# Performance work log

Hardware: AMD Instinct MI355X
Metric: run time of the kernel (lower is better)

The kernel has to match this reference:

```python
import jax, jax.numpy as jnp
import numpy as np

B = 1
H_IMG, W_IMG = 64, 64
NF = H_IMG * W_IMG          # 4096 front/query tokens
NS = 1024                   # satellite tokens (32x32 grid)
SAT_IN, FRONT_IN = 768, 320
NH, HD = 8, 64
MD = NH * HD                # 512
GHID, GHD = 128, 16
GMD = NH * GHD              # 128
GEO_RATIO, ROPE_BASE = 0.5, 10000.0
LAMBDA_GEO, LAMBDA_GEOM = 1.0, 1.0
EPS = 1e-5


def _linear(x, w, b):
    return x @ w.T + b


def _layernorm(x, g, b):
    m = x.mean(-1, keepdims=True)
    v = jnp.var(x, axis=-1, keepdims=True)
    return (x - m) / jnp.sqrt(v + EPS) * g + b


def _georope(t, xy):
    """Continuous 2D (x,y) rotary embedding on the first GEO_RATIO fraction of head_dim.
    t: [B,NH,N,HD], xy: [B,N,2]."""
    rot = int(HD * GEO_RATIO)       # rotated dims (32)
    axis = rot // 2                 # dims per spatial axis (16)
    half = axis // 2                # frequency pairs per axis (8)
    inv_freq = ROPE_BASE ** (-jnp.arange(half, dtype=t.dtype) / half)

    def rot_axis(a, coord):
        th = coord[:, None, :, None] * inv_freq   # [B,1,N,half]
        c, s = jnp.cos(th), jnp.sin(th)
        a1, a2 = a[..., :half], a[..., half:]
        return jnp.concatenate([a1 * c - a2 * s, a1 * s + a2 * c], axis=-1)

    tx = rot_axis(t[..., :axis], xy[..., 0])
    ty = rot_axis(t[..., axis:rot], xy[..., 1])
    return jnp.concatenate([tx, ty, t[..., rot:]], axis=-1)


def _heads(x, hd):
    b, n, _ = x.shape
    return x.reshape(b, n, NH, hd).transpose(0, 2, 1, 3)


def setup_inputs() -> dict:
    key = jax.random.key(0)
    ks = iter(jax.random.split(key, 64))

    def w(*shape):
        return jax.random.normal(next(ks), shape, jnp.float32) / np.sqrt(shape[-1]).astype(np.float32)

    z = lambda n: jnp.zeros((n,), jnp.float32)
    o = lambda n: jnp.ones((n,), jnp.float32)
    return {
        "front_feat": jax.random.normal(next(ks), (B, FRONT_IN, H_IMG, W_IMG), jnp.float32),
        "front_bev_xy": jax.random.uniform(next(ks), (B, NF, 2), jnp.float32, -1.0, 1.0),
        "sat_tokens": jax.random.normal(next(ks), (B, NS, SAT_IN), jnp.float32),
        "sat_xy": jax.random.uniform(next(ks), (B, NS, 2), jnp.float32, -1.0, 1.0),
        "front_plucker": jax.random.normal(next(ks), (B, NF, 6), jnp.float32),
        "pos_w1": w(MD, 2), "pos_b1": z(MD), "pos_w2": w(MD, MD), "pos_b2": z(MD),
        "fa_w": w(MD, FRONT_IN), "fa_b": z(MD), "fa_ln_g": o(MD), "fa_ln_b": z(MD),
        "qn_g": o(MD), "qn_b": z(MD),
        "sa_w": w(MD, SAT_IN), "sa_b": z(MD), "sa_ln_g": o(MD), "sa_ln_b": z(MD),
        "wq": w(MD, MD), "bq": z(MD), "wk": w(MD, MD), "bk": z(MD), "wv": w(MD, MD), "bv": z(MD),
        "plk_w1": w(GHID, 6), "plk_b1": z(GHID), "plk_w2": w(GHID, GHID), "plk_b2": z(GHID),
        "sxy_w1": w(GHID, 2), "sxy_b1": z(GHID), "sxy_w2": w(GHID, GHID), "sxy_b2": z(GHID),
        "gqn_g": o(GHID), "gqn_b": z(GHID), "gkn_g": o(GHID), "gkn_b": z(GHID),
        "wqg": w(GMD, GHID), "bqg": z(GMD), "wkg": w(GMD, GHID), "bkg": z(GMD),
    }


def reference(front_feat, front_bev_xy, sat_tokens, sat_xy, front_plucker,
              pos_w1, pos_b1, pos_w2, pos_b2, fa_w, fa_b, fa_ln_g, fa_ln_b,
              qn_g, qn_b, sa_w, sa_b, sa_ln_g, sa_ln_b, wq, bq, wk, bk, wv, bv,
              plk_w1, plk_b1, plk_w2, plk_b2, sxy_w1, sxy_b1, sxy_w2, sxy_b2,
              gqn_g, gqn_b, gkn_g, gkn_b, wqg, bqg, wkg, bkg):
    b = front_feat.shape[0]
    ff = front_feat.reshape(b, FRONT_IN, NF).transpose(0, 2, 1)      # [B,NF,C]
    pos = _linear(jax.nn.silu(_linear(front_bev_xy, pos_w1, pos_b1)), pos_w2, pos_b2)
    feat = _layernorm(_linear(ff, fa_w, fa_b), fa_ln_g, fa_ln_b)
    q_embed = _layernorm(pos + feat, qn_g, qn_b)
    sat_feat = _layernorm(_linear(sat_tokens, sa_w, sa_b), sa_ln_g, sa_ln_b)
    q = _heads(_linear(q_embed, wq, bq), HD)                         # [B,H,NF,HD]
    k = _heads(_linear(sat_feat, wk, bk), HD)                        # [B,H,NS,HD]
    v = _heads(_linear(sat_feat, wv, bv), HD)
    qr = _georope(q, front_bev_xy)
    kr = _georope(k, sat_xy)
    logits = jnp.einsum('bhqd,bhkd->bhqk', qr, kr) / np.float32(np.sqrt(HD))
    # learned geometric Q/K stream (Plucker rays vs sat xy)
    plk = _layernorm(_linear(jax.nn.silu(_linear(front_plucker, plk_w1, plk_b1)), plk_w2, plk_b2), gqn_g, gqn_b)
    sgf = _layernorm(_linear(jax.nn.silu(_linear(sat_xy, sxy_w1, sxy_b1)), sxy_w2, sxy_b2), gkn_g, gkn_b)
    qg = _heads(_linear(plk, wqg, bqg), GHD)
    kg = _heads(_linear(sgf, wkg, bkg), GHD)
    logits = logits + LAMBDA_GEOM * (jnp.einsum('bhqd,bhkd->bhqk', qg, kg) / np.float32(np.sqrt(GHD)))
    # additive pairwise squared-distance bias, broadcast over heads
    dist2 = ((front_bev_xy[:, :, None, :] - sat_xy[:, None, :, :]) ** 2).sum(-1)   # [B,NF,NS]
    logits = logits - LAMBDA_GEO * dist2[:, None]
    attn = jax.nn.softmax(logits, axis=-1)
    read = jnp.einsum('bhqk,bhkd->bhqd', attn, v)
    return read.transpose(0, 2, 1, 3).reshape(b, NF, MD)
```

## Files before the change

### kernel.cpp

```cpp
#include <hip/hip_runtime.h>
#include <hip/hip_bf16.h>
#include <stdint.h>

#define NF 4096
#define NS 1024
#define MD 512
#define HD 64
#define DA 96
#define GHID 128

#define L2E 1.44269504f
#define S2L 1.6986436f
#define SMAX 12.0f

typedef unsigned short u16;
typedef __attribute__((ext_vector_type(8))) short bf8v;
typedef __attribute__((ext_vector_type(4))) float f4v;

__device__ __forceinline__ u16 f2bf(float f) {
  __hip_bfloat16 h = __float2bfloat16(f);
  return __builtin_bit_cast(u16, h);
}
__device__ __forceinline__ float bf2f(u16 u) {
  union { unsigned u; float f; } v; v.u = ((unsigned)u) << 16; return v.f;
}
__device__ __forceinline__ f4v mfma16(bf8v a, bf8v b, f4v c) {
  return __builtin_amdgcn_mfma_f32_16x16x32_bf16(a, b, c, 0, 0, 0);
}
__device__ __forceinline__ void gld16(const void* g, void* l) {
  __builtin_amdgcn_global_load_lds(
      (const __attribute__((address_space(1))) unsigned int*)g,
      (__attribute__((address_space(3))) unsigned int*)l, 16, 0, 0);
}

#define OFF_POSW2 0
#define OFF_FAW   262144
#define OFF_SAW   425984
#define OFF_WQ    819200
#define OFF_WKV   1081344
#define OFF_PLKW2 1605632
#define OFF_SXYW2 1622016
#define OFF_WQG   1638400
#define OFF_WKG   1654784
#define OFF_SATT  1671168
#define TOTW      2457600

__global__ __launch_bounds__(256) void k_l0(
    const float* __restrict__ s0, const float* __restrict__ s1,
    const float* __restrict__ s2, const float* __restrict__ s3,
    const float* __restrict__ s4, const float* __restrict__ s5,
    const float* __restrict__ s6, const float* __restrict__ s7,
    const float* __restrict__ s8, const float* __restrict__ s9,
    const float* __restrict__ s10, u16* __restrict__ pool,
    const float* __restrict__ bk, const float* __restrict__ bv,
    float* __restrict__ bkv,
    const float* __restrict__ ff, u16* __restrict__ ffT,
    const float* __restrict__ in0, const float* __restrict__ w0,
    const float* __restrict__ b0, u16* __restrict__ o0,
    const float* __restrict__ in1, const float* __restrict__ w1,
    const float* __restrict__ b1, u16* __restrict__ o1,
    const float* __restrict__ in2, const float* __restrict__ w2,
    const float* __restrict__ b2, u16* __restrict__ o2) {
  __shared__ u16 sT[32][72];
  int blk = blockIdx.x, t = threadIdx.x;
  if (blk < 2401) {
    int i4 = blk * 256 + t;
    if (i4 < TOTW / 4) {
      int idx = i4 * 4;
      const float* src; int off;
      if      (idx < OFF_FAW)   { src = s0;  off = OFF_POSW2; }
      else if (idx < OFF_SAW)   { src = s1;  off = OFF_FAW; }
      else if (idx < OFF_WQ)    { src = s2;  off = OFF_SAW; }
      else if (idx < OFF_WKV)   { src = s3;  off = OFF_WQ; }
      else if (idx < 1343488)   { src = s4;  off = OFF_WKV; }
      else if (idx < OFF_PLKW2) { src = s5;  off = 1343488; }
      else if (idx < OFF_SXYW2) { src = s6;  off = OFF_PLKW2; }
      else if (idx < OFF_WQG)   { src = s7;  off = OFF_SXYW2; }
      else if (idx < OFF_WKG)   { src = s8;  off = OFF_WQG; }
      else if (idx < OFF_SATT)  { src = s9;  off = OFF_WKG; }
      else                      { src = s10; off = OFF_SATT; }
      float4 v = *(const float4*)(src + (idx - off));
      ushort4 o;
      o.x = f2bf(v.x); o.y = f2bf(v.y); o.z = f2bf(v.z); o.w = f2bf(v.w);
      *(ushort4*)(pool + idx) = o;
    } else if (i4 < TOTW / 4 + 256) {
      int j = (i4 - TOTW / 4) * 4;
#pragma unroll
      for (int e = 0; e < 4; ++e) {
        int b = j + e;
        bkv[b] = (b < 512) ? bk[b] : bv[b - 512];
      }
    }
  } else if (blk < 3041) {
    int lb = blk - 2401;
    int n0 = (lb & 63) * 64, c0 = (lb >> 6) * 32;
    {
      int cr = t >> 3, nc = (t & 7) * 8;
      const float* src = ff + (size_t)(c0 + cr) * NF + n0 + nc;
      float4 v0 = *(const float4*)src, v1 = *(const float4*)(src + 4);
      bf8v p;
      p[0]=(short)f2bf(v0.x); p[1]=(short)f2bf(v0.y); p[2]=(short)f2bf(v0.z); p[3]=(short)f2bf(v0.w);
      p[4]=(short)f2bf(v1.x); p[5]=(short)f2bf(v1.y); p[6]=(short)f2bf(v1.z); p[7]=(short)f2bf(v1.w);
      *(bf8v*)&sT[cr][nc] = p;
    }
    __syncthreads();
    {
      int r = t >> 2, cc = (t & 3) * 8;
      bf8v p;
#pragma unroll
      for (int e = 0; e < 8; ++e) p[e] = (short)sT[cc + e][r];
      *(bf8v*)(ffT + (size_t)(n0 + r) * 320 + c0 + cc) = p;
    }
  } else {
    int lb = blk - 3041;
    const float *in, *w, *b; u16* o; int mlog, K, idx;
    if (lb < 8192)       { in = in0; w = w0; b = b0; o = o0; mlog = 9; K = 2; idx = lb * 256 + t; }
    else if (lb < 10240) { in = in1; w = w1; b = b1; o = o1; mlog = 7; K = 6; idx = (lb - 8192) * 256 + t; }
    else                 { in = in2; w = w2; b = b2; o = o2; mlog = 7; K = 2; idx = (lb - 10240) * 256 + t; }
    int M = 1 << mlog;
    int n = idx >> mlog, m = idx & (M - 1);
    float acc = b[m];
    for (int k = 0; k < K; ++k) acc += in[n * K + k] * w[m * K + k];
    o[idx] = f2bf(acc / (1.f + __expf(-acc)));
  }
}

__device__ __forceinline__ void gemm_body(const u16* __restrict__ A, const u16* __restrict__ W,
                                          const float* __restrict__ bias, u16* __restrict__ out,
                                          int m0, int n0, int N, int K) {
  constexpr int BM = 64, BN = 64;
  constexpr int MR = 2, NR = 2;
  __shared__ u16 sA[2][BM * 64];
  __shared__ u16 sB[2][BN * 64];
  const int tid = threadIdx.x, w = tid >> 6, lane = tid & 63;
  const int l16 = lane & 15, lh = lane >> 4;
  const int wr = w >> 1, wc = w & 1;

  f4v acc[MR][NR];
#pragma unroll
  for (int m = 0; m < MR; ++m)
#pragma unroll
    for (int j = 0; j < NR; ++j) acc[m][j] = (f4v){0.f, 0.f, 0.f, 0.f};

  auto stageA = [&](int buf, int k0) {
#pragma unroll
    for (int i = 0; i < 2; ++i) {
      int c = i * 256 + tid;
      int row = c >> 3, cp = c & 7;
      int sc_ = cp ^ (row & 7);
      gld16(A + (size_t)(m0 + row) * K + k0 + sc_ * 8, &sA[buf][c * 8]);
    }
  };
  auto stageB = [&](int buf, int k0) {
#pragma unroll
    for (int i = 0; i < 2; ++i) {
      int c = i * 256 + tid;
      int row = c >> 3, cp = c & 7;
      int sc_ = cp ^ (row & 7);
      gld16(W + (size_t)(n0 + row) * K + k0 + sc_ * 8, &sB[buf][c * 8]);
    }
  };

  stageA(0, 0); stageB(0, 0);
  __syncthreads();
  const int NK = K >> 6;
  for (int ks = 0; ks < NK; ++ks) {
    int nb = ks & 1;
    if (ks + 1 < NK) { stageA(nb ^ 1, (ks + 1) * 64); stageB(nb ^ 1, (ks + 1) * 64); }
#pragma unroll
    for (int kk = 0; kk < 2; ++kk) {
      bf8v af[MR], bfr[NR];
#pragma unroll
      for (int m = 0; m < MR; ++m) {
        int row = wr * 32 + m * 16 + l16;
        int cp = (kk * 4 + lh) ^ (row & 7);
        af[m] = *(const bf8v*)&sA[nb][row * 64 + cp * 8];
      }
#pragma unroll
      for (int j = 0; j < NR; ++j) {
        int row = wc * 32 + j * 16 + l16;
        int cp = (kk * 4 + lh) ^ (row & 7);
        bfr[j] = *(const bf8v*)&sB[nb][row * 64 + cp * 8];
      }
#pragma unroll
      for (int m = 0; m < MR; ++m)
#pragma unroll
        for (int j = 0; j < NR; ++j) acc[m][j] = mfma16(af[m], bfr[j], acc[m][j]);
    }
    __syncthreads();
  }
#pragma unroll
  for (int m = 0; m < MR; ++m) {
    int grow = m0 + wr * 32 + m * 16 + (lh << 2);
#pragma unroll
    for (int j = 0; j < NR; ++j) {
      int gcol = n0 + wc * 32 + j * 16 + l16;
      float bv = bias ? bias[gcol] : 0.f;
#pragma unroll
      for (int r = 0; r < 4; ++r)
        out[(size_t)(grow + r) * N + gcol] = f2bf(acc[m][j][r] + bv);
    }
  }
}

struct GP { const u16* A; const u16* W; const float* bias; u16* out; int K; int N; int M; };

__device__ __forceinline__ void gemm_dispatch(const GP& g, int blk) {
  int mt = g.M >> 6;
  int m0 = (blk % mt) * 64, n0 = (blk / mt) * 64;
  gemm_body(g.A, g.W, g.bias, g.out, m0, n0, g.N, g.K);
}

__global__ __launch_bounds__(256) void k_gemm_L1(GP a, GP b, GP c, GP d, GP e) {
  int blk = blockIdx.x;
  if (blk < 512)       gemm_dispatch(a, blk);
  else if (blk < 1024) gemm_dispatch(b, blk - 512);
  else if (blk < 1152) gemm_dispatch(c, blk - 1024);
  else if (blk < 1280) gemm_dispatch(d, blk - 1152);
  else                 gemm_dispatch(e, blk - 1280);
}
__global__ __launch_bounds__(256) void k_gemm_L2(GP a, GP b, GP c, GP d) {
  int blk = blockIdx.x;
  if (blk < 512)      gemm_dispatch(a, blk);
  else if (blk < 768) gemm_dispatch(b, blk - 512);
  else if (blk < 896) gemm_dispatch(c, blk - 768);
  else                gemm_dispatch(d, blk - 896);
}

__global__ __launch_bounds__(256) void k_ln_all(
    const u16* __restrict__ feat_pre, const u16* __restrict__ pos,
    const float* __restrict__ fg, const float* __restrict__ fb,
    const float* __restrict__ qg, const float* __restrict__ qb2,
    u16* __restrict__ q_embed,
    const u16* __restrict__ satf_pre, const float* __restrict__ sg,
    const float* __restrict__ sb, u16* __restrict__ satf,
    const u16* __restrict__ ginq, const u16* __restrict__ gink,
    const float* __restrict__ ggq, const float* __restrict__ gbq,
    const float* __restrict__ ggk, const float* __restrict__ gbk,
    u16* __restrict__ goutq, u16* __restrict__ goutk) {
  int blk = blockIdx.x;
  int w = threadIdx.x >> 6, lane = threadIdx.x & 63;
  if (blk < 1024) {
    int row = blk * 4 + w;
    bf8v v = *(const bf8v*)(feat_pre + (size_t)row * 512 + lane * 8);
    float x[8];
#pragma unroll
    for (int e = 0; e < 8; ++e) x[e] = bf2f((u16)v[e]);
    float s = 0.f, q = 0.f;
#pragma unroll
    for (int e = 0; e < 8; ++e) { s += x[e]; q += x[e] * x[e]; }
#pragma unroll
    for (int mm = 1; mm < 64; mm <<= 1) { s += __shfl_xor(s, mm); q += __shfl_xor(q, mm); }
    float mean = s / 512.f, var = q / 512.f - mean * mean;
    float rstd = rsqrtf(var + 1e-5f);
    bf8v vp = *(const bf8v*)(pos + (size_t)row * 512 + lane * 8);
#pragma unroll
    for (int e = 0; e < 8; ++e)
      x[e] = (x[e] - mean) * rstd * fg[lane * 8 + e] + fb[lane * 8 + e] + bf2f((u16)vp[e]);
    s = 0.f; q = 0.f;
#pragma unroll
    for (int e = 0; e < 8; ++e) { s += x[e]; q += x[e] * x[e]; }
#pragma unroll
    for (int mm = 1; mm < 64; mm <<= 1) { s += __shfl_xor(s, mm); q += __shfl_xor(q, mm); }
    mean = s / 512.f; var = q / 512.f - mean * mean;
    rstd = rsqrtf(var + 1e-5f);
    bf8v ov;
#pragma unroll
    for (int e = 0; e < 8; ++e)
      ov[e] = (short)f2bf((x[e] - mean) * rstd * qg[lane * 8 + e] + qb2[lane * 8 + e]);
    *(bf8v*)(q_embed + (size_t)row * 512 + lane * 8) = ov;
  } else if (blk < 1280) {
    int row = (blk - 1024) * 4 + w;
    bf8v v = *(const bf8v*)(satf_pre + (size_t)row * 512 + lane * 8);
    float x[8];
#pragma unroll
    for (int e = 0; e < 8; ++e) x[e] = bf2f((u16)v[e]);
    float s = 0.f, q = 0.f;
#pragma unroll
    for (int e = 0; e < 8; ++e) { s += x[e]; q += x[e] * x[e]; }
#pragma unroll
    for (int mm = 1; mm < 64; mm <<= 1) { s += __shfl_xor(s, mm); q += __shfl_xor(q, mm); }
    float mean = s / 512.f, var = q / 512.f - mean * mean;
    float rstd = rsqrtf(var + 1e-5f);
    bf8v ov;
#pragma unroll
    for (int e = 0; e < 8; ++e)
      ov[e] = (short)f2bf((x[e] - mean) * rstd * sg[lane * 8 + e] + sb[lane * 8 + e]);
    *(bf8v*)(satf + (size_t)row * 512 + lane * 8) = ov;
  } else {
    int row = (blk - 1280) * 4 + w;
    const u16* in; const float *g, *b; u16* out;
    if (row < 4096) { in = ginq; g = ggq; b = gbq; out = goutq; }
    else { row -= 4096; in = gink; g = ggk; b = gbk; out = goutk; }
    uint32_t v = *(const uint32_t*)(in + (size_t)row * 128 + lane * 2);
    float x0 = bf2f((u16)(v & 0xffff)), x1 = bf2f((u16)(v >> 16));
    float s = x0 + x1, q = x0 * x0 + x1 * x1;
#pragma unroll
    for (int mm = 1; mm < 64; mm <<= 1) { s += __shfl_xor(s, mm); q += __shfl_xor(q, mm); }
    float mean = s / 128.f, var = q / 128.f - mean * mean;
    float rstd = rsqrtf(var + 1e-5f);
    u16 o0 = f2bf((x0 - mean) * rstd * g[lane * 2] + b[lane * 2]);
    u16 o1 = f2bf((x1 - mean) * rstd * g[lane * 2 + 1] + b[lane * 2 + 1]);
    *(uint32_t*)(out + (size_t)row * 128 + lane * 2) = (uint32_t)o0 | ((uint32_t)o1 << 16);
  }
}

__global__ __launch_bounds__(256) void k_prep(
    const u16* __restrict__ qlin, const u16* __restrict__ qglin,
    const float* __restrict__ qxy, u16* __restrict__ Qaug_,
    const u16* __restrict__ klin, const u16* __restrict__ kglin,
    const float* __restrict__ kxy, u16* __restrict__ Kaug_,
    float* __restrict__ kk2_, u16* __restrict__ VT) {
  __shared__ u16 sT[64][72];
  int blk = blockIdx.x;
  if (blk < 10240) {
    int gid = blk * 4 + (threadIdx.x >> 6);
    int lane = threadIdx.x & 63;
    const u16 *lin, *glin; const float* xy; u16* aug;
    int lstride, n, h, isQ; float scm, scg;
    if (gid < NF * 8) {
      lin = qlin; glin = qglin; xy = qxy; aug = Qaug_;
      lstride = MD; n = gid >> 3; h = gid & 7; isQ = 1;
      scm = 0.125f * L2E; scg = 0.25f * L2E;
    } else {
      gid -= NF * 8;
      lin = klin; glin = kglin; xy = kxy; aug = Kaug_;
      lstride = 1024; n = gid >> 3; h = gid & 7; isQ = 0;
      scm = 1.f; scg = 1.f;
    }
    float val = bf2f(lin[(size_t)n * lstride + h * 64 + lane]);
    float part = __shfl_xor(val, 8);
    float x = xy[n * 2], y = xy[n * 2 + 1];
    float outv = val;
    if (lane < 32) {
      float coord = (lane < 16) ? x : y;
      int j = lane & 7;
      float th = coord * __expf(-(float)j * 1.1512925465f);
      float sn, cs;
      __sincosf(th, &sn, &cs);
      outv = ((lane & 8) == 0) ? (val * cs - part * sn) : (part * sn + val * cs);
    }
    u16* dst = aug + (size_t)(h * (isQ ? NF : NS) + n) * DA;
    dst[lane] = f2bf(outv * scm);
    if (lane < 16) {
      float gv = bf2f(glin[(size_t)n * GHID + h * 16 + lane]);
      dst[64 + lane] = f2bf(gv * scg);
    } else if (lane == 16) {
      dst[80] = f2bf(S2L * x);
    } else if (lane == 17) {
      dst[81] = f2bf(S2L * y);
    } else if (lane == 18) {
      dst[82] = 0;
      if (!isQ && h == 0) kk2_[n] = L2E * (x * x + y * y) + SMAX;
    } else if (lane < 32) {
      dst[64 + lane] = 0;
    }
  } else {
    int lb = blk - 10240;
    int n0 = (lb & 15) * 64, h = lb >> 4;
    int t = threadIdx.x;
    int r = t >> 2, c = (t & 3) * 16;
    const u16* src = klin + (size_t)(n0 + r) * 1024 + 512 + h * 64 + c;
    *(bf8v*)&sT[r][c]     = *(const bf8v*)src;
    *(bf8v*)&sT[r][c + 8] = *(const bf8v*)(src + 8);
    __syncthreads();
    int d = t >> 2, nc = (t & 3) * 16;
    bf8v p0, p1;
#pragma unroll
    for (int e = 0; e < 8; ++e) { p0[e] = (short)sT[nc + e][d]; p1[e] = (short)sT[nc + 8 + e][d]; }
    u16* dst = VT + (size_t)(h * 64 + d) * 1024 + n0 + nc;
    *(bf8v*)dst = p0;
    *(bf8v*)(dst + 8) = p1;
  }
}

__global__ __launch_bounds__(256, 4) void k_flash(const u16* __restrict__ Qa,
                                                  const u16* __restrict__ Ka,
                                                  const u16* __restrict__ VT,
                                                  const float* __restrict__ kk2,
                                                  float* __restrict__ Opart,
                                                  float* __restrict__ lbuf) {
  const int h = blockIdx.y, qb = blockIdx.x, sp = blockIdx.z;
  const int tid = threadIdx.x, w = tid >> 6, lane = tid & 63;
  const int l16 = lane & 15, lh = lane >> 4;
  __shared__ u16 sK[64][104];
  __shared__ u16 sV[64][72];
  __shared__ u16 sP[4][16][72];
  __shared__ float sKK[512];

  ((float2*)sKK)[tid] = ((const float2*)(kk2 + sp * 512))[tid];

  const int qrow = qb * 64 + w * 16 + l16;
  bf8v qf[3];
#pragma unroll
  for (int c = 0; c < 3; ++c)
    qf[c] = *(const bf8v*)(Qa + (size_t)(h * NF + qrow) * DA + c * 32 + lh * 8);

  bf8v ONES;
#pragma unroll
  for (int i = 0; i < 8; ++i) ONES[i] = (short)0x3F80;

  const int crow = qb * 64 + w * 16 + (lh << 2);
  float l_run[4] = {0.f, 0.f, 0.f, 0.f};
  f4v accO[4];
#pragma unroll
  for (int d = 0; d < 4; ++d) accO[d] = (f4v){0.f, 0.f, 0.f, 0.f};

  const int kt0 = sp * 8;
  bf8v kreg[3], vreg[2];
  auto sload = [&](int t8) {
    int kb = (kt0 + t8) * 64;
#pragma unroll
    for (int i = 0; i < 3; ++i) {
      int c = tid + i * 256; int r = c / 12, off = (c % 12) * 8;
      kreg[i] = *(const bf8v*)(Ka + ((size_t)(h * NS) + kb + r) * DA + off);
    }
#pragma unroll
    for (int i = 0; i < 2; ++i) {
      int c = tid + i * 256; int d = c >> 3, off = (c & 7) * 8;
      vreg[i] = *(const bf8v*)(VT + ((size_t)(h * HD) + d) * NS + kb + off);
    }
  };
  auto swrite = [&]() {
#pragma unroll
    for (int i = 0; i < 3; ++i) {
      int c = tid + i * 256; int r = c / 12, off = (c % 12) * 8;
      *(bf8v*)&sK[r][off] = kreg[i];
    }
#pragma unroll
    for (int i = 0; i < 2; ++i) {
      int c = tid + i * 256; int d = c >> 3, off = (c & 7) * 8;
      *(bf8v*)&sV[d][off] = vreg[i];
    }
  };

  sload(0); swrite();
  __syncthreads();
  for (int t8 = 0; t8 < 8; ++t8) {
    if (t8 < 7) sload(t8 + 1);
#pragma unroll
    for (int j = 0; j < 4; ++j) {
      f4v s4 = (f4v){0.f, 0.f, 0.f, 0.f};
#pragma unroll
      for (int c = 0; c < 3; ++c) {
        bf8v kf = *(const bf8v*)&sK[j * 16 + l16][c * 32 + lh * 8];
        s4 = mfma16(qf[c], kf, s4);
      }
      float ck = sKK[t8 * 64 + j * 16 + l16];
#pragma unroll
      for (int r = 0; r < 4; ++r) {
        float pv = exp2f(s4[r] - ck);
        sP[w][(lh << 2) + r][j * 16 + l16] = f2bf(pv);
      }
    }
    bf8v pf0 = *(const bf8v*)&sP[w][l16][lh * 8];
    bf8v pf1 = *(const bf8v*)&sP[w][l16][32 + lh * 8];
    f4v ls = (f4v){0.f, 0.f, 0.f, 0.f};
    ls = mfma16(pf0, ONES, ls);
    ls = mfma16(pf1, ONES, ls);
#pragma unroll
    for (int r = 0; r < 4; ++r) l_run[r] += ls[r];
#pragma unroll
    for (int c = 0; c < 2; ++c) {
      bf8v pf = (c == 0) ? pf0 : pf1;
#pragma unroll
      for (int d = 0; d < 4; ++d) {
        bf8v vf = *(const bf8v*)&sV[d * 16 + l16][c * 32 + lh * 8];
        accO[d] = mfma16(pf, vf, accO[d]);
      }
    }
    __syncthreads();
    if (t8 < 7) swrite();
    __syncthreads();
  }
  size_t obase = (size_t)(sp * 8 + h) * NF + crow;
#pragma unroll
  for (int d = 0; d < 4; ++d)
#pragma unroll
    for (int r = 0; r < 4; ++r)
      Opart[(obase + r) * 64 + d * 16 + l16] = accO[d][r];
  if (l16 == 0) {
#pragma unroll
    for (int r = 0; r < 4; ++r) lbuf[obase + r] = l_run[r];
  }
}

__global__ void k_combine(const float* __restrict__ Opart, const float* __restrict__ lbuf,
                          float* __restrict__ out) {
  int i4 = blockIdx.x * 256 + threadIdx.x;
  int n = i4 >> 7;
  int c4 = i4 & 127, h = c4 >> 4, d4 = c4 & 15;
  float l = lbuf[(size_t)h * NF + n] + lbuf[(size_t)(8 + h) * NF + n];
  float rl = 1.f / l;
  float4 o1 = ((const float4*)(Opart + ((size_t)h * NF + n) * 64))[d4];
  float4 o2 = ((const float4*)(Opart + ((size_t)(8 + h) * NF + n) * 64))[d4];
  float4 r;
  r.x = (o1.x + o2.x) * rl;
  r.y = (o1.y + o2.y) * rl;
  r.z = (o1.z + o2.z) * rl;
  r.w = (o1.w + o2.w) * rl;
  ((float4*)out)[i4] = r;
}

extern "C" void kernel_launch(void* const* d_in, const int* in_sizes, int n_in,
                              void* d_out, int out_size, void* d_ws, size_t ws_size,
                              hipStream_t stream) {
  (void)in_sizes; (void)n_in; (void)out_size; (void)ws_size;
  const float* front_feat = (const float*)d_in[0];
  const float* bev_xy     = (const float*)d_in[1];
  const float* sat_tokens = (const float*)d_in[2];
  const float* sat_xy     = (const float*)d_in[3];
  const float* plucker    = (const float*)d_in[4];
  const float* pos_w1 = (const float*)d_in[5];
  const float* pos_b1 = (const float*)d_in[6];
  const float* pos_w2 = (const float*)d_in[7];
  const float* pos_b2 = (const float*)d_in[8];
  const float* fa_w   = (const float*)d_in[9];
  const float* fa_b   = (const float*)d_in[10];
  const float* fa_ln_g = (const float*)d_in[11];
  const float* fa_ln_b = (const float*)d_in[12];
  const float* qn_g   = (const float*)d_in[13];
  const float* qn_b   = (const float*)d_in[14];
  const float* sa_w   = (const float*)d_in[15];
  const float* sa_b   = (const float*)d_in[16];
  const float* sa_ln_g = (const float*)d_in[17];
  const float* sa_ln_b = (const float*)d_in[18];
  const float* wq = (const float*)d_in[19];
  const float* bq = (const float*)d_in[20];
  const float* wk = (const float*)d_in[21];
  const float* bk = (const float*)d_in[22];
  const float* wv = (const float*)d_in[23];
  const float* bv = (const float*)d_in[24];
  const float* plk_w1 = (const float*)d_in[25];
  const float* plk_b1 = (const float*)d_in[26];
  const float* plk_w2 = (const float*)d_in[27];
  const float* plk_b2 = (const float*)d_in[28];
  const float* sxy_w1 = (const float*)d_in[29];
  const float* sxy_b1 = (const float*)d_in[30];
  const float* sxy_w2 = (const float*)d_in[31];
  const float* sxy_b2 = (const float*)d_in[32];
  const float* gqn_g = (const float*)d_in[33];
  const float* gqn_b = (const float*)d_in[34];
  const float* gkn_g = (const float*)d_in[35];
  const float* gkn_b = (const float*)d_in[36];
  const float* wqg = (const float*)d_in[37];
  const float* bqg = (const float*)d_in[38];
  const float* wkg = (const float*)d_in[39];
  const float* bkg = (const float*)d_in[40];

  char* ws = (char*)d_ws;
  size_t off = 0;
  auto alloc = [&](size_t bytes) {
    size_t r = off;
    off += (bytes + 255) & ~(size_t)255;
    return r;
  };
  u16*   wpool   = (u16*)(ws + alloc((size_t)TOTW * 2));
  float* bkv     = (float*)(ws + alloc(1024 * 4));
  u16*   ffT     = (u16*)(ws + alloc((size_t)NF * 320 * 2));
  u16*   pos_h   = (u16*)(ws + alloc((size_t)NF * MD * 2));
  u16*   plk_h   = (u16*)(ws + alloc((size_t)NF * GHID * 2));
  u16*   sxy_h   = (u16*)(ws + alloc((size_t)NS * GHID * 2));
  u16*   pos     = (u16*)(ws + alloc((size_t)NF * MD * 2));
  u16*   feat_pre= (u16*)(ws + alloc((size_t)NF * MD * 2));
  u16*   satf_pre= (u16*)(ws + alloc((size_t)NS * MD * 2));
  u16*   satf    = (u16*)(ws + alloc((size_t)NS * MD * 2));
  u16*   q_embed = (u16*)(ws + alloc((size_t)NF * MD * 2));
  u16*   plk2    = (u16*)(ws + alloc((size_t)NF * GHID * 2));
  u16*   sxy2    = (u16*)(ws + alloc((size_t)NS * GHID * 2));
  u16*   q_lin   = (u16*)(ws + alloc((size_t)NF * MD * 2));
  u16*   kv_lin  = (u16*)(ws + alloc((size_t)NS * 1024 * 2));
  u16*   Qaug    = (u16*)(ws + alloc((size_t)8 * NF * DA * 2));
  u16*   Kaug    = (u16*)(ws + alloc((size_t)8 * NS * DA * 2));
  u16*   VT      = (u16*)(ws + alloc((size_t)8 * HD * NS * 2));
  float* kk2     = (float*)(ws + alloc((size_t)NS * 4));
  float* Opart   = (float*)(ws + alloc((size_t)2 * 8 * NF * 64 * 4));
  float* lbuf    = (float*)(ws + alloc((size_t)2 * 8 * NF * 4));
  u16* plk_ln = plk_h;
  u16* sgf    = sxy_h;
  u16* qg_lin = plk2;
  u16* kg_lin = sxy2;

  dim3 b256(256);
  k_l0<<<dim3(13793), b256, 0, stream>>>(
      pos_w2, fa_w, sa_w, wq, wk, wv, plk_w2, sxy_w2, wqg, wkg, sat_tokens,
      wpool, bk, bv, bkv, front_feat, ffT,
      bev_xy, pos_w1, pos_b1, pos_h,
      plucker, plk_w1, plk_b1, plk_h,
      sat_xy, sxy_w1, sxy_b1, sxy_h);

  GP gpos {pos_h, wpool + OFF_POSW2, pos_b2, pos, 512, 512, 4096};
  GP gfeat{ffT, wpool + OFF_FAW, fa_b, feat_pre, 320, 512, 4096};
  GP gsat {wpool + OFF_SATT, wpool + OFF_SAW, sa_b, satf_pre, 768, 512, 1024};
  GP ggq1 {plk_h, wpool + OFF_PLKW2, plk_b2, plk2, 128, 128, 4096};
  GP ggk1 {sxy_h, wpool + OFF_SXYW2, sxy_b2, sxy2, 128, 128, 1024};
  k_gemm_L1<<<dim3(1312), b256, 0, stream>>>(gpos, gfeat, gsat, ggq1, ggk1);

  k_ln_all<<<dim3(2560), b256, 0, stream>>>(
      feat_pre, pos, fa_ln_g, fa_ln_b, qn_g, qn_b, q_embed,
      satf_pre, sa_ln_g, sa_ln_b, satf,
      plk2, sxy2, gqn_g, gqn_b, gkn_g, gkn_b, plk_ln, sgf);

  GP gq  {q_embed, wpool + OFF_WQ, bq, q_lin, 512, 512, 4096};
  GP gkv {satf, wpool + OFF_WKV, bkv, kv_lin, 512, 1024, 1024};
  GP ggq2{plk_ln, wpool + OFF_WQG, bqg, qg_lin, 128, 128, 4096};
  GP ggk2{sgf, wpool + OFF_WKG, bkg, kg_lin, 128, 128, 1024};
  k_gemm_L2<<<dim3(928), b256, 0, stream>>>(gq, gkv, ggq2, ggk2);

  k_prep<<<dim3(10368), b256, 0, stream>>>(
      q_lin, qg_lin, bev_xy, Qaug, kv_lin, kg_lin, sat_xy, Kaug, kk2, VT);

  k_flash<<<dim3(NF / 64, 8, 2), b256, 0, stream>>>(Qaug, Kaug, VT, kk2, Opart, lbuf);
  k_combine<<<dim3(NF * MD / 4 / 256), b256, 0, stream>>>(Opart, lbuf, (float*)d_out);
}
```

Baseline: 87.01 us.

## Fuse RoPE/Qaug/Kaug/VT prep into GEMM epilogues and store split-K partials in bf16

Removes the k_prep kernel. The geo-rope rotation, scaling, Qaug/Kaug packing and the V transpose now happen directly in the L2 GEMM epilogues, and the constant xy/zero columns plus kk2 are written by extra blocks in the first kernel. This drops one launch and the round trip of the q_lin/kv_lin intermediates through memory. Separately, the flash kernel's split partial outputs are stored as bf16 instead of fp32, which halves combine traffic but loses some precision. The epilogue stores become scattered, with per-element writes into strided aug buffers.

Result: faster. 79.76 us (-8.3%).

```diff
diff --git a/kernel.cpp b/kernel.cpp
--- a/kernel.cpp
+++ b/kernel.cpp
@@ -44,6 +44,11 @@
 #define OFF_WKG   1654784
 #define OFF_SATT  1671168
 #define TOTW      2457600
+
+#define EPI_OUT  0
+#define EPI_ROPE 1
+#define EPI_VT   2
+#define EPI_GEO  3
 
 __global__ __launch_bounds__(256) void k_l0(
     const float* __restrict__ s0, const float* __restrict__ s1,
@@ -60,7 +65,8 @@
     const float* __restrict__ in1, const float* __restrict__ w1,
     const float* __restrict__ b1, u16* __restrict__ o1,
     const float* __restrict__ in2, const float* __restrict__ w2,
-    const float* __restrict__ b2, u16* __restrict__ o2) {
+    const float* __restrict__ b2, u16* __restrict__ o2,
+    u16* __restrict__ Qaug, u16* __restrict__ Kaug, float* __restrict__ kk2) {
   __shared__ u16 sT[32][72];
   int blk = blockIdx.x, t = threadIdx.x;
   if (blk < 2401) {
@@ -111,7 +117,7 @@
       for (int e = 0; e < 8; ++e) p[e] = (short)sT[cc + e][r];
       *(bf8v*)(ffT + (size_t)(n0 + r) * 320 + c0 + cc) = p;
     }
-  } else {
+  } else if (blk < 13793) {
     int lb = blk - 3041;
     const float *in, *w, *b; u16* o; int mlog, K, idx;
     if (lb < 8192)       { in = in0; w = w0; b = b0; o = o0; mlog = 9; K = 2; idx = lb * 256 + t; }
@@ -122,16 +128,35 @@
     float acc = b[m];
     for (int k = 0; k < K; ++k) acc += in[n * K + k] * w[m * K + k];
     o[idx] = f2bf(acc / (1.f + __expf(-acc)));
+  } else {
+    int id = (blk - 13793) * 256 + t;
+    int side = id >= NF * 8;
+    int lid = side ? id - NF * 8 : id;
+    int n = lid >> 3, h = lid & 7;
+    const float* xy = side ? in2 : in0;
+    u16* aug = side ? Kaug : Qaug;
+    int nrows = side ? NS : NF;
+    float x = xy[n * 2], y = xy[n * 2 + 1];
+    bf8v p0, z;
+#pragma unroll
+    for (int e = 0; e < 8; ++e) { p0[e] = 0; z[e] = 0; }
+    p0[0] = (short)f2bf(S2L * x);
+    p0[1] = (short)f2bf(S2L * y);
+    u16* dst = aug + ((size_t)h * nrows + n) * DA + 80;
+    *(bf8v*)dst = p0;
+    *(bf8v*)(dst + 8) = z;
+    if (side && h == 0) kk2[n] = L2E * (x * x + y * y) + SMAX;
   }
 }
 
 __device__ __forceinline__ void gemm_body(const u16* __restrict__ A, const u16* __restrict__ W,
                                           const float* __restrict__ bias, u16* __restrict__ out,
-                                          int m0, int n0, int N, int K) {
-  constexpr int BM = 64, BN = 64;
+                                          int m0, int n0, int N, int K,
+                                          int mode, float scale, const float* __restrict__ xy,
+                                          u16* __restrict__ aug, int nrows) {
   constexpr int MR = 2, NR = 2;
-  __shared__ u16 sA[2][BM * 64];
-  __shared__ u16 sB[2][BN * 64];
+  __shared__ u16 sA[2][64 * 64];
+  __shared__ u16 sB[2][64 * 64];
   const int tid = threadIdx.x, w = tid >> 6, lane = tid & 63;
   const int l16 = lane & 15, lh = lane >> 4;
   const int wr = w >> 1, wc = w & 1;
@@ -189,26 +214,91 @@
     }
     __syncthreads();
   }
-#pragma unroll
-  for (int m = 0; m < MR; ++m) {
-    int grow = m0 + wr * 32 + m * 16 + (lh << 2);
-#pragma unroll
-    for (int j = 0; j < NR; ++j) {
-      int gcol = n0 + wc * 32 + j * 16 + l16;
-      float bv = bias ? bias[gcol] : 0.f;
-#pragma unroll
-      for (int r = 0; r < 4; ++r)
-        out[(size_t)(grow + r) * N + gcol] = f2bf(acc[m][j][r] + bv);
+
+  if (mode == EPI_OUT) {
+#pragma unroll
+    for (int m = 0; m < MR; ++m) {
+      int grow = m0 + wr * 32 + m * 16 + (lh << 2);
+#pragma unroll
+      for (int j = 0; j < NR; ++j) {
+        int gcol = n0 + wc * 32 + j * 16 + l16;
+        float bvs = bias ? bias[gcol] : 0.f;
+#pragma unroll
+        for (int r = 0; r < 4; ++r)
+          out[(size_t)(grow + r) * N + gcol] = f2bf(acc[m][j][r] + bvs);
+      }
+    }
+  } else if (mode == EPI_ROPE) {
+    float fr = __expf(-(float)(l16 & 7) * 1.1512925465f);
+#pragma unroll
+    for (int m = 0; m < MR; ++m) {
+      int grow = m0 + wr * 32 + m * 16 + (lh << 2);
+#pragma unroll
+      for (int j = 0; j < NR; ++j) {
+        int gcol = n0 + wc * 32 + j * 16 + l16;
+        int h = gcol >> 6, d = gcol & 63;
+        float bvs = bias[gcol];
+#pragma unroll
+        for (int r = 0; r < 4; ++r) {
+          int n = grow + r;
+          float val = acc[m][j][r] + bvs;
+          float part = __shfl_xor(val, 8);
+          float outv = val;
+          if (wc == 0) {
+            float2 c2 = ((const float2*)xy)[n];
+            float coord = j ? c2.y : c2.x;
+            float sn, cs;
+            __sincosf(coord * fr, &sn, &cs);
+            outv = (l16 & 8) ? (part * sn + val * cs) : (val * cs - part * sn);
+          }
+          aug[((size_t)h * nrows + n) * DA + d] = f2bf(outv * scale);
+        }
+      }
+    }
+  } else if (mode == EPI_VT) {
+#pragma unroll
+    for (int m = 0; m < MR; ++m) {
+      int grow = m0 + wr * 32 + m * 16 + (lh << 2);
+#pragma unroll
+      for (int j = 0; j < NR; ++j) {
+        int gcol = n0 + wc * 32 + j * 16 + l16;
+        int vcol = gcol - 512;
+        int h = vcol >> 6, d = vcol & 63;
+        float bvs = bias[gcol];
+        ushort4 o;
+        o.x = f2bf(acc[m][j][0] + bvs);
+        o.y = f2bf(acc[m][j][1] + bvs);
+        o.z = f2bf(acc[m][j][2] + bvs);
+        o.w = f2bf(acc[m][j][3] + bvs);
+        *(ushort4*)(aug + ((size_t)(h * 64 + d)) * NS + grow) = o;
+      }
+    }
+  } else {
+#pragma unroll
+    for (int m = 0; m < MR; ++m) {
+      int grow = m0 + wr * 32 + m * 16 + (lh << 2);
+#pragma unroll
+      for (int j = 0; j < NR; ++j) {
+        int gcol = n0 + wc * 32 + j * 16 + l16;
+        int h = gcol >> 4, dg = gcol & 15;
+        float bvs = bias[gcol];
+#pragma unroll
+        for (int r = 0; r < 4; ++r)
+          aug[((size_t)h * nrows + grow + r) * DA + 64 + dg] = f2bf((acc[m][j][r] + bvs) * scale);
+      }
     }
   }
 }
 
-struct GP { const u16* A; const u16* W; const float* bias; u16* out; int K; int N; int M; };
+struct GP { const u16* A; const u16* W; const float* bias; u16* out;
+            int K; int N; int M; int mode; float scale; const float* xy;
+            u16* aug; int nrows; };
 
 __device__ __forceinline__ void gemm_dispatch(const GP& g, int blk) {
   int mt = g.M >> 6;
   int m0 = (blk % mt) * 64, n0 = (blk / mt) * 64;
-  gemm_body(g.A, g.W, g.bias, g.out, m0, n0, g.N, g.K);
+  gemm_body(g.A, g.W, g.bias, g.out, m0, n0, g.N, g.K,
+            g.mode, g.scale, g.xy, g.aug, g.nrows);
 }
 
 __global__ __launch_bounds__(256) void k_gemm_L1(GP a, GP b, GP c, GP d, GP e) {
@@ -219,12 +309,22 @@
   else if (blk < 1280) gemm_dispatch(d, blk - 1152);
   else                 gemm_dispatch(e, blk - 1280);
 }
-__global__ __launch_bounds__(256) void k_gemm_L2(GP a, GP b, GP c, GP d) {
+__global__ __launch_bounds__(256) void k_gemm_L2(GP a, GP b, GP c, GP d, u16* VTp) {
   int blk = blockIdx.x;
-  if (blk < 512)      gemm_dispatch(a, blk);
-  else if (blk < 768) gemm_dispatch(b, blk - 512);
-  else if (blk < 896) gemm_dispatch(c, blk - 768);
-  else                gemm_dispatch(d, blk - 896);
+  if (blk < 512) {
+    gemm_dispatch(a, blk);
+  } else if (blk < 768) {
+    int lb = blk - 512;
+    int m0 = (lb & 15) * 64, n0 = (lb >> 4) * 64;
+    if (n0 >= 512)
+      gemm_body(b.A, b.W, b.bias, b.out, m0, n0, b.N, b.K, EPI_VT, 1.f, nullptr, VTp, NS);
+    else
+      gemm_body(b.A, b.W, b.bias, b.out, m0, n0, b.N, b.K, b.mode, b.scale, b.xy, b.aug, b.nrows);
+  } else if (blk < 896) {
+    gemm_dispatch(c, blk - 768);
+  } else {
+    gemm_dispatch(d, blk - 896);
+  }
 }
 
 __global__ __launch_bounds__(256) void k_ln_all(
@@ -305,80 +405,11 @@
   }
 }
 
-__global__ __launch_bounds__(256) void k_prep(
-    const u16* __restrict__ qlin, const u16* __restrict__ qglin,
-    const float* __restrict__ qxy, u16* __restrict__ Qaug_,
-    const u16* __restrict__ klin, const u16* __restrict__ kglin,
-    const float* __restrict__ kxy, u16* __restrict__ Kaug_,
-    float* __restrict__ kk2_, u16* __restrict__ VT) {
-  __shared__ u16 sT[64][72];
-  int blk = blockIdx.x;
-  if (blk < 10240) {
-    int gid = blk * 4 + (threadIdx.x >> 6);
-    int lane = threadIdx.x & 63;
-    const u16 *lin, *glin; const float* xy; u16* aug;
-    int lstride, n, h, isQ; float scm, scg;
-    if (gid < NF * 8) {
-      lin = qlin; glin = qglin; xy = qxy; aug = Qaug_;
-      lstride = MD; n = gid >> 3; h = gid & 7; isQ = 1;
-      scm = 0.125f * L2E; scg = 0.25f * L2E;
-    } else {
-      gid -= NF * 8;
-      lin = klin; glin = kglin; xy = kxy; aug = Kaug_;
-      lstride = 1024; n = gid >> 3; h = gid & 7; isQ = 0;
-      scm = 1.f; scg = 1.f;
-    }
-    float val = bf2f(lin[(size_t)n * lstride + h * 64 + lane]);
-    float part = __shfl_xor(val, 8);
-    float x = xy[n * 2], y = xy[n * 2 + 1];
-    float outv = val;
-    if (lane < 32) {
-      float coord = (lane < 16) ? x : y;
-      int j = lane & 7;
-      float th = coord * __expf(-(float)j * 1.1512925465f);
-      float sn, cs;
-      __sincosf(th, &sn, &cs);
-      outv = ((lane & 8) == 0) ? (val * cs - part * sn) : (part * sn + val * cs);
-    }
-    u16* dst = aug + (size_t)(h * (isQ ? NF : NS) + n) * DA;
-    dst[lane] = f2bf(outv * scm);
-    if (lane < 16) {
-      float gv = bf2f(glin[(size_t)n * GHID + h * 16 + lane]);
-      dst[64 + lane] = f2bf(gv * scg);
-    } else if (lane == 16) {
-      dst[80] = f2bf(S2L * x);
-    } else if (lane == 17) {
-      dst[81] = f2bf(S2L * y);
-    } else if (lane == 18) {
-      dst[82] = 0;
-      if (!isQ && h == 0) kk2_[n] = L2E * (x * x + y * y) + SMAX;
-    } else if (lane < 32) {
-      dst[64 + lane] = 0;
-    }
-  } else {
-    int lb = blk - 10240;
-    int n0 = (lb & 15) * 64, h = lb >> 4;
-    int t = threadIdx.x;
-    int r = t >> 2, c = (t & 3) * 16;
-    const u16* src = klin + (size_t)(n0 + r) * 1024 + 512 + h * 64 + c;
-    *(bf8v*)&sT[r][c]     = *(const bf8v*)src;
-    *(bf8v*)&sT[r][c + 8] = *(const bf8v*)(src + 8);
-    __syncthreads();
-    int d = t >> 2, nc = (t & 3) * 16;
-    bf8v p0, p1;
-#pragma unroll
-    for (int e = 0; e < 8; ++e) { p0[e] = (short)sT[nc + e][d]; p1[e] = (short)sT[nc + 8 + e][d]; }
-    u16* dst = VT + (size_t)(h * 64 + d) * 1024 + n0 + nc;
-    *(bf8v*)dst = p0;
-    *(bf8v*)(dst + 8) = p1;
-  }
-}
-
 __global__ __launch_bounds__(256, 4) void k_flash(const u16* __restrict__ Qa,
                                                   const u16* __restrict__ Ka,
                                                   const u16* __restrict__ VT,
                                                   const float* __restrict__ kk2,
-                                                  float* __restrict__ Opart,
+                                                  u16* __restrict__ Opart,
                                                   float* __restrict__ lbuf) {
   const int h = blockIdx.y, qb = blockIdx.x, sp = blockIdx.z;
   const int tid = threadIdx.x, w = tid >> 6, lane = tid & 63;
@@ -478,27 +509,27 @@
   for (int d = 0; d < 4; ++d)
 #pragma unroll
     for (int r = 0; r < 4; ++r)
-      Opart[(obase + r) * 64 + d * 16 + l16] = accO[d][r];
+      Opart[(obase + r) * 64 + d * 16 + l16] = f2bf(accO[d][r]);
   if (l16 == 0) {
 #pragma unroll
     for (int r = 0; r < 4; ++r) lbuf[obase + r] = l_run[r];
   }
 }
 
-__global__ void k_combine(const float* __restrict__ Opart, const float* __restrict__ lbuf,
+__global__ void k_combine(const u16* __restrict__ Opart, const float* __restrict__ lbuf,
                           float* __restrict__ out) {
   int i4 = blockIdx.x * 256 + threadIdx.x;
   int n = i4 >> 7;
   int c4 = i4 & 127, h = c4 >> 4, d4 = c4 & 15;
   float l = lbuf[(size_t)h * NF + n] + lbuf[(size_t)(8 + h) * NF + n];
   float rl = 1.f / l;
-  float4 o1 = ((const float4*)(Opart + ((size_t)h * NF + n) * 64))[d4];
-  float4 o2 = ((const float4*)(Opart + ((size_t)(8 + h) * NF + n) * 64))[d4];
+  ushort4 a = ((const ushort4*)(Opart + ((size_t)h * NF + n) * 64))[d4];
+  ushort4 b = ((const ushort4*)(Opart + ((size_t)(8 + h) * NF + n) * 64))[d4];
   float4 r;
-  r.x = (o1.x + o2.x) * rl;
-  r.y = (o1.y + o2.y) * rl;
-  r.z = (o1.z + o2.z) * rl;
-  r.w = (o1.w + o2.w) * rl;
+  r.x = (bf2f(a.x) + bf2f(b.x)) * rl;
+  r.y = (bf2f(a.y) + bf2f(b.y)) * rl;
+  r.z = (bf2f(a.z) + bf2f(b.z)) * rl;
+  r.w = (bf2f(a.w) + bf2f(b.w)) * rl;
   ((float4*)out)[i4] = r;
 }
 
@@ -568,32 +599,29 @@
   u16*   q_embed = (u16*)(ws + alloc((size_t)NF * MD * 2));
   u16*   plk2    = (u16*)(ws + alloc((size_t)NF * GHID * 2));
   u16*   sxy2    = (u16*)(ws + alloc((size_t)NS * GHID * 2));
-  u16*   q_lin   = (u16*)(ws + alloc((size_t)NF * MD * 2));
-  u16*   kv_lin  = (u16*)(ws + alloc((size_t)NS * 1024 * 2));
   u16*   Qaug    = (u16*)(ws + alloc((size_t)8 * NF * DA * 2));
   u16*   Kaug    = (u16*)(ws + alloc((size_t)8 * NS * DA * 2));
   u16*   VT      = (u16*)(ws + alloc((size_t)8 * HD * NS * 2));
   float* kk2     = (float*)(ws + alloc((size_t)NS * 4));
-  float* Opart   = (float*)(ws + alloc((size_t)2 * 8 * NF * 64 * 4));
+  u16*   Opart   = (u16*)(ws + alloc((size_t)2 * 8 * NF * 64 * 2));
   float* lbuf    = (float*)(ws + alloc((size_t)2 * 8 * NF * 4));
   u16* plk_ln = plk_h;
   u16* sgf    = sxy_h;
-  u16* qg_lin = plk2;
-  u16* kg_lin = sxy2;
 
   dim3 b256(256);
-  k_l0<<<dim3(13793), b256, 0, stream>>>(
+  k_l0<<<dim3(13953), b256, 0, stream>>>(
       pos_w2, fa_w, sa_w, wq, wk, wv, plk_w2, sxy_w2, wqg, wkg, sat_tokens,
       wpool, bk, bv, bkv, front_feat, ffT,
       bev_xy, pos_w1, pos_b1, pos_h,
       plucker, plk_w1, plk_b1, plk_h,
-      sat_xy, sxy_w1, sxy_b1, sxy_h);
-
-  GP gpos {pos_h, wpool + OFF_POSW2, pos_b2, pos, 512, 512, 4096};
-  GP gfeat{ffT, wpool + OFF_FAW, fa_b, feat_pre, 320, 512, 4096};
-  GP gsat {wpool + OFF_SATT, wpool + OFF_SAW, sa_b, satf_pre, 768, 512, 1024};
-  GP ggq1 {plk_h, wpool + OFF_PLKW2, plk_b2, plk2, 128, 128, 4096};
-  GP ggk1 {sxy_h, wpool + OFF_SXYW2, sxy_b2, sxy2, 128, 128, 1024};
+      sat_xy, sxy_w1, sxy_b1, sxy_h,
+      Qaug, Kaug, kk2);
+
+  GP gpos {pos_h, wpool + OFF_POSW2, pos_b2, pos, 512, 512, 4096, EPI_OUT, 0.f, nullptr, nullptr, 0};
+  GP gfeat{ffT, wpool + OFF_FAW, fa_b, feat_pre, 320, 512, 4096, EPI_OUT, 0.f, nullptr, nullptr, 0};
+  GP gsat {wpool + OFF_SATT, wpool + OFF_SAW, sa_b, satf_pre, 768, 512, 1024, EPI_OUT, 0.f, nullptr, nullptr, 0};
+  GP ggq1 {plk_h, wpool + OFF_PLKW2, plk_b2, plk2, 128, 128, 4096, EPI_OUT, 0.f, nullptr, nullptr, 0};
+  GP ggk1 {sxy_h, wpool + OFF_SXYW2, sxy_b2, sxy2, 128, 128, 1024, EPI_OUT, 0.f, nullptr, nullptr, 0};
   k_gemm_L1<<<dim3(1312), b256, 0, stream>>>(gpos, gfeat, gsat, ggq1, ggk1);
 
   k_ln_all<<<dim3(2560), b256, 0, stream>>>(
@@ -601,14 +629,11 @@
       satf_pre, sa_ln_g, sa_ln_b, satf,
       plk2, sxy2, gqn_g, gqn_b, gkn_g, gkn_b, plk_ln, sgf);
 
-  GP gq  {q_embed, wpool + OFF_WQ, bq, q_lin, 512, 512, 4096};
-  GP gkv {satf, wpool + OFF_WKV, bkv, kv_lin, 512, 1024, 1024};
-  GP ggq2{plk_ln, wpool + OFF_WQG, bqg, qg_lin, 128, 128, 4096};
-  GP ggk2{sgf, wpool + OFF_WKG, bkg, kg_lin, 128, 128, 1024};
-  k_gemm_L2<<<dim3(928), b256, 0, stream>>>(gq, gkv, ggq2, ggk2);
-
-  k_prep<<<dim3(10368), b256, 0, stream>>>(
-      q_lin, qg_lin, bev_xy, Qaug, kv_lin, kg_lin, sat_xy, Kaug, kk2, VT);
+  GP gq  {q_embed, wpool + OFF_WQ, bq, nullptr, 512, 512, 4096, EPI_ROPE, 0.125f * L2E, bev_xy, Qaug, NF};
+  GP gkv {satf, wpool + OFF_WKV, bkv, nullptr, 512, 1024, 1024, EPI_ROPE, 1.f, sat_xy, Kaug, NS};
+  GP ggq2{plk_ln, wpool + OFF_WQG, bqg, nullptr, 128, 128, 4096, EPI_GEO, 0.25f * L2E, nullptr, Qaug, NF};
+  GP ggk2{sgf, wpool + OFF_WKG, bkg, nullptr, 128, 128, 1024, EPI_GEO, 1.f, nullptr, Kaug, NS};
+  k_gemm_L2<<<dim3(928), b256, 0, stream>>>(gq, gkv, ggq2, ggk2, VT);
 
   k_flash<<<dim3(NF / 64, 8, 2), b256, 0, stream>>>(Qaug, Kaug, VT, kk2, Opart, lbuf);
   k_combine<<<dim3(NF * MD / 4 / 256), b256, 0, stream>>>(Opart, lbuf, (float*)d_out);
```
